# Kernel optimization log

Measured on AMD Instinct MI355X. Metric: run time of the kernel, lower is better.

Reference implementation:

```python
import jax, jax.numpy as jnp
import numpy as np


def crf_log_likelihood(logits, tags, mask, transitions, start_trans, end_trans):
    """AllenNLP-style linear-chain CRF log-likelihood, summed over the batch.
    logits: [B,T,K] float, tags: [B,T] int, mask: [B,T] float (1=valid).
    include_start_end_transitions=True.
    """
    B, T, K = logits.shape
    lt = jnp.transpose(logits, (1, 0, 2))          # [T,B,K]
    mt = jnp.transpose(mask, (1, 0))               # [T,B]
    tt = jnp.transpose(tags, (1, 0))               # [T,B]

    # ---- partition function (forward algorithm) ----
    alpha0 = start_trans + lt[0]                   # [B,K]

    def part_step(alpha, xs):
        emit, m = xs                               # emit [B,K], m [B]
        # inner[b,i,j] = alpha[b,i] + transitions[i,j] + emit[b,j]
        inner = alpha[:, :, None] + emit[:, None, :] + transitions[None, :, :]
        new_alpha = jax.nn.logsumexp(inner, axis=1)
        alpha = new_alpha * m[:, None] + alpha * (1.0 - m[:, None])
        return alpha, None

    alpha, _ = jax.lax.scan(part_step, alpha0, (lt[1:], mt[1:]))
    log_denominator = jax.nn.logsumexp(alpha + end_trans, axis=1)  # [B]

    # ---- joint (gold-path) score ----
    score0 = start_trans[tt[0]]                    # [B]

    def joint_step(score, xs):
        cur, nxt, emit, m_cur, m_nxt = xs
        trans_s = transitions[cur, nxt]                                   # [B]
        emit_s = jnp.take_along_axis(emit, cur[:, None], axis=1)[:, 0]    # [B]
        return score + trans_s * m_nxt + emit_s * m_cur, None

    score, _ = jax.lax.scan(joint_step, score0,
                            (tt[:-1], tt[1:], lt[:-1], mt[:-1], mt[1:]))
    last_idx = (jnp.sum(mt, axis=0) - 1.0).astype(jnp.int32)              # [B]
    last_tags = tt[last_idx, jnp.arange(B)]                               # [B]
    last_emit = jnp.take_along_axis(lt[-1], last_tags[:, None], axis=1)[:, 0]
    score = score + end_trans[last_tags] + last_emit * mt[-1]
    return jnp.sum(score - log_denominator)


def setup_inputs() -> dict:
    key = jax.random.key(0)
    ks = jax.random.split(key, 6)
    B, T, D, K = 64, 512, 768, 21
    vectors = jax.random.normal(ks[0], (B, T, D), dtype=jnp.float32)
    targets = jax.random.randint(ks[1], (B, T), 0, K, dtype=jnp.int32)
    mask = jnp.ones((B, T), dtype=jnp.int32)
    # Linear(input_dim, n_classes)
    W = jax.random.normal(ks[2], (K, D), dtype=jnp.float32) * (1.0 / np.sqrt(D))
    b = jax.random.normal(ks[3], (K,), dtype=jnp.float32) * 0.01
    transitions = jax.random.normal(ks[4], (K, K), dtype=jnp.float32) * 0.1
    se = jax.random.normal(ks[5], (2, K), dtype=jnp.float32) * 0.1
    return {"vectors": vectors, "targets": targets, "mask": mask,
            "W": W, "b": b, "transitions": transitions,
            "start_trans": se[0], "end_trans": se[1]}


def reference(vectors, targets, mask, W, b, transitions, start_trans, end_trans):
    logits = jnp.einsum('btd,kd->btk', vectors, W) + b     # proj
    maskf = mask.astype(logits.dtype)
    ll = crf_log_likelihood(logits, targets, maskf, transitions, start_trans, end_trans)
    loss = -ll / jnp.sum(maskf)
    return loss, logits
```

## Files before the change

### kernel.cpp

```cpp
#include <hip/hip_runtime.h>

#define B_ 64
#define T_ 512
#define D_ 768
#define K_ 21
#define NCHUNK 32
#define CLEN 16
#define GSTRIDE 448
#define LOG21 3.0445224377234229965f

__global__ __launch_bounds__(512) void proj_kernel(
    const float* __restrict__ A,
    const float* __restrict__ W,
    const float* __restrict__ bias,
    float* __restrict__ out)
{
    __shared__ float Wl[K_ * D_];
    const int tid = threadIdx.x;
    {
        const float4* Wg = (const float4*)W;
        float4* Ws = (float4*)Wl;
        for (int i = tid; i < K_ * D_ / 4; i += 512) Ws[i] = Wg[i];
    }
    __syncthreads();

    const int m = tid & 15;
    const size_t row = (size_t)blockIdx.x * 32 + (tid >> 4);
    const float4* __restrict__ Arow = (const float4*)(A + row * D_);
    const float4* __restrict__ Wl4 = (const float4*)Wl;

    float acc[K_];
    #pragma unroll
    for (int k = 0; k < K_; ++k) acc[k] = 0.0f;

    #pragma unroll 4
    for (int i = 0; i < 12; ++i) {
        const float4 a = Arow[m + 16 * i];
        #pragma unroll
        for (int k = 0; k < K_; ++k) {
            const float4 w = Wl4[k * 192 + m + 16 * i];
            acc[k] = fmaf(a.x, w.x, fmaf(a.y, w.y, fmaf(a.z, w.z, fmaf(a.w, w.w, acc[k]))));
        }
    }

    #pragma unroll
    for (int k = 0; k < K_; ++k) {
        float v = acc[k];
        v += __shfl_xor(v, 1, 64);
        v += __shfl_xor(v, 2, 64);
        v += __shfl_xor(v, 4, 64);
        v += __shfl_xor(v, 8, 64);
        acc[k] = v;
    }

    float* o = out + 1 + row * K_;
    #pragma unroll
    for (int k = 0; k < K_; ++k) {
        if (m == (k & 15)) o[k] = acc[k] + bias[k];
    }
}

__global__ __launch_bounds__(64) void chunk_kernel(
    const float* __restrict__ outF,
    const int*   __restrict__ mask,
    const float* __restrict__ trans,
    float* __restrict__ G,
    float* __restrict__ SC)
{
    __shared__ float M0[441], M1[441];
    __shared__ float sET[441];
    __shared__ float em[CLEN * K_];
    __shared__ float smx[CLEN];
    __shared__ int   smask[CLEN];

    const int c = blockIdx.x;
    const int b = blockIdx.y;
    const int lane = threadIdx.x;
    const int t0 = c * CLEN + 1;
    const int nst = min(CLEN, T_ - t0);
    const int i_ = lane / 3;
    const int jg = lane - i_ * 3;
    const bool act = lane < 63;

    const float* lg = outF + 1 + (size_t)b * T_ * K_;
    for (int idx = lane; idx < nst * K_; idx += 64) em[idx] = lg[t0 * K_ + idx];
    if (lane < nst) smask[lane] = mask[b * T_ + t0 + lane];
    for (int idx = lane; idx < 441; idx += 64) {
        M0[idx] = (idx % 22 == 0) ? 1.0f : 0.0f;
        sET[idx] = __expf(trans[idx]);
    }
    __syncthreads();

    if (lane < nst) {
        float mx = -1e30f;
        for (int j = 0; j < K_; ++j) mx = fmaxf(mx, em[lane * K_ + j]);
        smx[lane] = mx;
    }
    __syncthreads();
    for (int idx = lane; idx < nst * K_; idx += 64)
        em[idx] = __expf(em[idx] - smx[idx / K_]) * (1.0f / 21.0f);

    float ETc[K_ * 7];
    if (act) {
        #pragma unroll
        for (int mm = 0; mm < K_; ++mm) {
            #pragma unroll
            for (int q = 0; q < 7; ++q)
                ETc[mm * 7 + q] = sET[mm * K_ + jg * 7 + q];
        }
    }
    __syncthreads();

    int cur = 0;
    for (int s = 0; s < nst; ++s) {
        if (smask[s] != 0) {
            const float* Mr = cur ? M1 : M0;
            float*       Mw = cur ? M0 : M1;
            float facc[7] = {0.f,0.f,0.f,0.f,0.f,0.f,0.f};
            if (act) {
                #pragma unroll
                for (int mm = 0; mm < K_; ++mm) {
                    const float lm = Mr[i_ * K_ + mm];
                    #pragma unroll
                    for (int q = 0; q < 7; ++q)
                        facc[q] = fmaf(lm, ETc[mm * 7 + q], facc[q]);
                }
            }
            __syncthreads();
            if (act) {
                #pragma unroll
                for (int q = 0; q < 7; ++q)
                    Mw[i_ * K_ + jg * 7 + q] = facc[q] * em[s * K_ + jg * 7 + q];
            }
            __syncthreads();
            cur ^= 1;
        }
    }

    float* Gc = G + (size_t)(b * NCHUNK + c) * GSTRIDE;
    const float* Mf = cur ? M1 : M0;
    for (int idx = lane; idx < 441; idx += 64) Gc[idx] = Mf[idx];
    if (lane == 0) {
        float sc = 0.0f;
        for (int s = 0; s < nst; ++s)
            if (smask[s] != 0) sc += smx[s] + LOG21;
        SC[b * NCHUNK + c] = sc;
    }
}

__global__ __launch_bounds__(64) void scan_kernel(
    const float* __restrict__ outF,
    const int*   __restrict__ tags,
    const int*   __restrict__ mask,
    const float* __restrict__ trans,
    const float* __restrict__ startT,
    const float* __restrict__ endT,
    const float* __restrict__ G,
    const float* __restrict__ SC,
    float* __restrict__ ll,
    float* __restrict__ msum)
{
    __shared__ float sG[2][GSTRIDE];
    __shared__ float sv[24];
    __shared__ float sm[T_];
    __shared__ int   st[T_];
    const int b = blockIdx.x;
    const int lane = threadIdx.x;
    const int jc = min(lane, K_ - 1);
    const float* lg = outF + 1 + (size_t)b * T_ * K_;
    const float* Gb = G + (size_t)b * NCHUNK * GSTRIDE;

    for (int t = lane; t < T_; t += 64) {
        sm[t] = (float)mask[b * T_ + t];
        st[t] = tags[b * T_ + t];
    }
    const float scv = (lane < NCHUNK) ? SC[b * NCHUNK + lane] : 0.0f;

    {
        const float4* Gf4 = (const float4*)Gb;
        float4* dst = (float4*)sG[0];
        dst[lane] = Gf4[lane];
        if (lane < 48) dst[lane + 64] = Gf4[lane + 64];
    }

    float val = (lane < K_) ? startT[lane] + lg[lane] : -1e30f;
    float mx = val;
    #pragma unroll
    for (int off = 32; off >= 1; off >>= 1) mx = fmaxf(mx, __shfl_xor(mx, off, 64));
    float v = (lane < K_) ? __expf(val - mx) : 0.0f;
    float C = mx;

    for (int c = 0; c < NCHUNK; ++c) {
        if (lane < K_) sv[lane] = v;
        __syncthreads();

        float4 p0, p1;
        const bool have = (c + 1) < NCHUNK;
        if (have) {
            const float4* Gf4 = (const float4*)(Gb + (size_t)(c + 1) * GSTRIDE);
            p0 = Gf4[lane];
            if (lane < 48) p1 = Gf4[lane + 64];
        }

        const float* Gc = sG[c & 1];
        float a0 = 0.f, a1 = 0.f, a2 = 0.f;
        #pragma unroll
        for (int i = 0; i < K_; i += 3) {
            a0 = fmaf(sv[i],     Gc[i * K_ + jc],       a0);
            a1 = fmaf(sv[i + 1], Gc[(i + 1) * K_ + jc], a1);
            a2 = fmaf(sv[i + 2], Gc[(i + 2) * K_ + jc], a2);
        }
        const float s = a0 + a1 + a2;
        C += __shfl(scv, c, 64);
        float m2 = (lane < K_) ? s : 0.0f;
        #pragma unroll
        for (int off = 32; off >= 1; off >>= 1) m2 = fmaxf(m2, __shfl_xor(m2, off, 64));
        v = (lane < K_) ? s / m2 : 0.0f;
        C += __logf(m2);

        if (have) {
            float4* dst = (float4*)sG[(c + 1) & 1];
            dst[lane] = p0;
            if (lane < 48) dst[lane + 64] = p1;
        }
        __syncthreads();
    }

    float term = (lane < K_) ? v * __expf(endT[lane]) : 0.0f;
    #pragma unroll
    for (int off = 32; off >= 1; off >>= 1) term += __shfl_xor(term, off, 64);
    const float logZ = C + __logf(term);

    float sc = 0.0f, ms = 0.0f;
    for (int t = lane; t < T_; t += 64) {
        const float mt = sm[t];
        ms += mt;
        if (t < T_ - 1) {
            const int ct = st[t], nt2 = st[t + 1];
            sc += trans[ct * K_ + nt2] * sm[t + 1] + lg[t * K_ + ct] * mt;
        }
    }
    #pragma unroll
    for (int off = 32; off >= 1; off >>= 1) {
        sc += __shfl_xor(sc, off, 64);
        ms += __shfl_xor(ms, off, 64);
    }
    if (lane == 0) {
        const int lastIdx = (int)ms - 1;
        const int lastTag = st[lastIdx];
        sc += startT[st[0]] + endT[lastTag] + lg[(T_ - 1) * K_ + lastTag] * sm[T_ - 1];
        ll[b]   = sc - logZ;
        msum[b] = ms;
    }
}

__global__ __launch_bounds__(64) void crf_kernel(
    const float* __restrict__ outF,
    const int*   __restrict__ tags,
    const int*   __restrict__ mask,
    const float* __restrict__ trans,
    const float* __restrict__ startT,
    const float* __restrict__ endT,
    float* __restrict__ ws)
{
    __shared__ float se[T_ * K_];
    __shared__ float sm[T_];
    __shared__ int   st[T_];
    const int b = blockIdx.x;
    const int lane = threadIdx.x;

    const float* lg = outF + 1 + (size_t)b * T_ * K_;
    for (int i = lane; i < T_ * K_; i += 64) se[i] = lg[i];
    for (int t = lane; t < T_; t += 64) {
        sm[t] = (float)mask[b * T_ + t];
        st[t] = tags[b * T_ + t];
    }
    __syncthreads();

    const int jc = lane < K_ ? lane : K_ - 1;
    float ET[K_];
    #pragma unroll
    for (int i = 0; i < K_; ++i) ET[i] = __expf(trans[i * K_ + jc]);

    float a0   = startT[jc] + se[jc];
    float r0   = __shfl(a0, 0, 64);
    float aRel = a0 - r0;
    float C    = r0;

    for (int t = 1; t < T_; ++t) {
        if (sm[t] != 0.0f) {
            float e = __expf(aRel);
            float s = 0.0f;
            #pragma unroll
            for (int i = 0; i < K_; ++i)
                s = fmaf(__shfl(e, i, 64), ET[i], s);
            float raw = __logf(s) + se[t * K_ + jc];
            float rr  = __shfl(raw, 0, 64);
            aRel = raw - rr;
            C   += rr;
        }
    }

    float contrib = (lane < K_) ? __expf(aRel + endT[jc]) : 0.0f;
    #pragma unroll
    for (int off = 32; off >= 1; off >>= 1) contrib += __shfl_xor(contrib, off, 64);
    const float logZ = C + __logf(contrib);

    float sc = 0.0f, ms = 0.0f;
    for (int t = lane; t < T_; t += 64) {
        const float mt = sm[t];
        ms += mt;
        if (t < T_ - 1) {
            const int ct = st[t], nt2 = st[t + 1];
            sc += trans[ct * K_ + nt2] * sm[t + 1] + se[t * K_ + ct] * mt;
        }
    }
    #pragma unroll
    for (int off = 32; off >= 1; off >>= 1) {
        sc += __shfl_xor(sc, off, 64);
        ms += __shfl_xor(ms, off, 64);
    }
    if (lane == 0) {
        const int lastIdx = (int)ms - 1;
        const int lastTag = st[lastIdx];
        sc += startT[st[0]] + endT[lastTag] + se[(T_ - 1) * K_ + lastTag] * sm[T_ - 1];
        ws[b]      = sc - logZ;
        ws[B_ + b] = ms;
    }
}

__global__ __launch_bounds__(64) void fin_kernel(
    const float* __restrict__ ll, const float* __restrict__ msum,
    float* __restrict__ outF)
{
    const int lane = threadIdx.x;
    float l = ll[lane];
    float m = msum[lane];
    #pragma unroll
    for (int off = 32; off >= 1; off >>= 1) {
        l += __shfl_xor(l, off, 64);
        m += __shfl_xor(m, off, 64);
    }
    if (lane == 0) outF[0] = -l / m;
}

extern "C" void kernel_launch(void* const* d_in, const int* in_sizes, int n_in,
                              void* d_out, int out_size, void* d_ws, size_t ws_size,
                              hipStream_t stream) {
    const float* A     = (const float*)d_in[0];
    const int*   tags  = (const int*)  d_in[1];
    const int*   mask  = (const int*)  d_in[2];
    const float* W     = (const float*)d_in[3];
    const float* bias  = (const float*)d_in[4];
    const float* trans = (const float*)d_in[5];
    const float* stT   = (const float*)d_in[6];
    const float* enT   = (const float*)d_in[7];
    float* outF = (float*)d_out;
    float* ws   = (float*)d_ws;

    proj_kernel<<<1024, 512, 0, stream>>>(A, W, bias, outF);

    const size_t gFloats  = (size_t)B_ * NCHUNK * GSTRIDE;
    const size_t scOff    = gFloats;
    const size_t llOff    = gFloats + (size_t)B_ * NCHUNK;
    const size_t msOff    = llOff + B_;
    const size_t needBytes = (msOff + B_) * sizeof(float);

    if (ws_size >= needBytes) {
        float* G   = ws;
        float* SC  = ws + scOff;
        float* llp = ws + llOff;
        float* msv = ws + msOff;
        chunk_kernel<<<dim3(NCHUNK, B_), 64, 0, stream>>>(outF, mask, trans, G, SC);
        scan_kernel<<<B_, 64, 0, stream>>>(outF, tags, mask, trans, stT, enT, G, SC, llp, msv);
        fin_kernel<<<1, 64, 0, stream>>>(llp, msv, outF);
    } else {
        crf_kernel<<<B_, 64, 0, stream>>>(outF, tags, mask, trans, stT, enT, ws);
        fin_kernel<<<1, 64, 0, stream>>>(ws, ws + B_, outF);
    }
}
```

Baseline: 218.3 us.

## Compute four rows per thread in projection and preload all chunk matrices in scan

```diff
diff --git a/kernel.cpp b/kernel.cpp
--- a/kernel.cpp
+++ b/kernel.cpp
@@ -25,38 +25,61 @@
     __syncthreads();
 
     const int m = tid & 15;
-    const size_t row = (size_t)blockIdx.x * 32 + (tid >> 4);
-    const float4* __restrict__ Arow = (const float4*)(A + row * D_);
+    const int rid = tid >> 4;
+    const size_t row0 = (size_t)blockIdx.x * 128 + rid;
+    const float4* __restrict__ Ar0 = (const float4*)(A + (row0      ) * D_);
+    const float4* __restrict__ Ar1 = (const float4*)(A + (row0 + 32 ) * D_);
+    const float4* __restrict__ Ar2 = (const float4*)(A + (row0 + 64 ) * D_);
+    const float4* __restrict__ Ar3 = (const float4*)(A + (row0 + 96 ) * D_);
     const float4* __restrict__ Wl4 = (const float4*)Wl;
 
-    float acc[K_];
-    #pragma unroll
-    for (int k = 0; k < K_; ++k) acc[k] = 0.0f;
-
-    #pragma unroll 4
+    float acc0[K_], acc1[K_], acc2[K_], acc3[K_];
+    #pragma unroll
+    for (int k = 0; k < K_; ++k) { acc0[k]=0.f; acc1[k]=0.f; acc2[k]=0.f; acc3[k]=0.f; }
+
+    #pragma unroll 2
     for (int i = 0; i < 12; ++i) {
-        const float4 a = Arow[m + 16 * i];
+        const float4 a0 = Ar0[m + 16 * i];
+        const float4 a1 = Ar1[m + 16 * i];
+        const float4 a2 = Ar2[m + 16 * i];
+        const float4 a3 = Ar3[m + 16 * i];
         #pragma unroll
         for (int k = 0; k < K_; ++k) {
             const float4 w = Wl4[k * 192 + m + 16 * i];
-            acc[k] = fmaf(a.x, w.x, fmaf(a.y, w.y, fmaf(a.z, w.z, fmaf(a.w, w.w, acc[k]))));
+            acc0[k] = fmaf(a0.x, w.x, fmaf(a0.y, w.y, fmaf(a0.z, w.z, fmaf(a0.w, w.w, acc0[k]))));
+            acc1[k] = fmaf(a1.x, w.x, fmaf(a1.y, w.y, fmaf(a1.z, w.z, fmaf(a1.w, w.w, acc1[k]))));
+            acc2[k] = fmaf(a2.x, w.x, fmaf(a2.y, w.y, fmaf(a2.z, w.z, fmaf(a2.w, w.w, acc2[k]))));
+            acc3[k] = fmaf(a3.x, w.x, fmaf(a3.y, w.y, fmaf(a3.z, w.z, fmaf(a3.w, w.w, acc3[k]))));
         }
     }
 
     #pragma unroll
     for (int k = 0; k < K_; ++k) {
-        float v = acc[k];
-        v += __shfl_xor(v, 1, 64);
-        v += __shfl_xor(v, 2, 64);
-        v += __shfl_xor(v, 4, 64);
-        v += __shfl_xor(v, 8, 64);
-        acc[k] = v;
-    }
-
-    float* o = out + 1 + row * K_;
+        float v0 = acc0[k], v1 = acc1[k], v2 = acc2[k], v3 = acc3[k];
+        v0 += __shfl_xor(v0, 1, 64); v1 += __shfl_xor(v1, 1, 64);
+        v2 += __shfl_xor(v2, 1, 64); v3 += __shfl_xor(v3, 1, 64);
+        v0 += __shfl_xor(v0, 2, 64); v1 += __shfl_xor(v1, 2, 64);
+        v2 += __shfl_xor(v2, 2, 64); v3 += __shfl_xor(v3, 2, 64);
+        v0 += __shfl_xor(v0, 4, 64); v1 += __shfl_xor(v1, 4, 64);
+        v2 += __shfl_xor(v2, 4, 64); v3 += __shfl_xor(v3, 4, 64);
+        v0 += __shfl_xor(v0, 8, 64); v1 += __shfl_xor(v1, 8, 64);
+        v2 += __shfl_xor(v2, 8, 64); v3 += __shfl_xor(v3, 8, 64);
+        acc0[k] = v0; acc1[k] = v1; acc2[k] = v2; acc3[k] = v3;
+    }
+
+    float* o0 = out + 1 + (row0      ) * K_;
+    float* o1 = out + 1 + (row0 + 32 ) * K_;
+    float* o2 = out + 1 + (row0 + 64 ) * K_;
+    float* o3 = out + 1 + (row0 + 96 ) * K_;
     #pragma unroll
     for (int k = 0; k < K_; ++k) {
-        if (m == (k & 15)) o[k] = acc[k] + bias[k];
+        if (m == (k & 15)) {
+            const float bb = bias[k];
+            o0[k] = acc0[k] + bb;
+            o1[k] = acc1[k] + bb;
+            o2[k] = acc2[k] + bb;
+            o3[k] = acc3[k] + bb;
+        }
     }
 }
 
@@ -160,7 +183,7 @@
     float* __restrict__ ll,
     float* __restrict__ msum)
 {
-    __shared__ float sG[2][GSTRIDE];
+    __shared__ float sG[NCHUNK * GSTRIDE];
     __shared__ float sv[24];
     __shared__ float sm[T_];
     __shared__ int   st[T_];
@@ -170,39 +193,29 @@
     const float* lg = outF + 1 + (size_t)b * T_ * K_;
     const float* Gb = G + (size_t)b * NCHUNK * GSTRIDE;
 
+    {
+        const float4* Gf4 = (const float4*)Gb;
+        float4* dst = (float4*)sG;
+        for (int j = lane; j < NCHUNK * GSTRIDE / 4; j += 64) dst[j] = Gf4[j];
+    }
     for (int t = lane; t < T_; t += 64) {
         sm[t] = (float)mask[b * T_ + t];
         st[t] = tags[b * T_ + t];
     }
     const float scv = (lane < NCHUNK) ? SC[b * NCHUNK + lane] : 0.0f;
 
-    {
-        const float4* Gf4 = (const float4*)Gb;
-        float4* dst = (float4*)sG[0];
-        dst[lane] = Gf4[lane];
-        if (lane < 48) dst[lane + 64] = Gf4[lane + 64];
-    }
-
     float val = (lane < K_) ? startT[lane] + lg[lane] : -1e30f;
     float mx = val;
     #pragma unroll
     for (int off = 32; off >= 1; off >>= 1) mx = fmaxf(mx, __shfl_xor(mx, off, 64));
     float v = (lane < K_) ? __expf(val - mx) : 0.0f;
     float C = mx;
+    __syncthreads();
 
     for (int c = 0; c < NCHUNK; ++c) {
         if (lane < K_) sv[lane] = v;
         __syncthreads();
-
-        float4 p0, p1;
-        const bool have = (c + 1) < NCHUNK;
-        if (have) {
-            const float4* Gf4 = (const float4*)(Gb + (size_t)(c + 1) * GSTRIDE);
-            p0 = Gf4[lane];
-            if (lane < 48) p1 = Gf4[lane + 64];
-        }
-
-        const float* Gc = sG[c & 1];
+        const float* Gc = sG + c * GSTRIDE;
         float a0 = 0.f, a1 = 0.f, a2 = 0.f;
         #pragma unroll
         for (int i = 0; i < K_; i += 3) {
@@ -217,12 +230,6 @@
         for (int off = 32; off >= 1; off >>= 1) m2 = fmaxf(m2, __shfl_xor(m2, off, 64));
         v = (lane < K_) ? s / m2 : 0.0f;
         C += __logf(m2);
-
-        if (have) {
-            float4* dst = (float4*)sG[(c + 1) & 1];
-            dst[lane] = p0;
-            if (lane < 48) dst[lane + 64] = p1;
-        }
         __syncthreads();
     }
 
@@ -358,7 +365,7 @@
     float* outF = (float*)d_out;
     float* ws   = (float*)d_ws;
 
-    proj_kernel<<<1024, 512, 0, stream>>>(A, W, bias, outF);
+    proj_kernel<<<256, 512, 0, stream>>>(A, W, bias, outF);
 
     const size_t gFloats  = (size_t)B_ * NCHUNK * GSTRIDE;
     const size_t scOff    = gFloats;
```

Result: slower. 231.9 us (+6.2%).
